# Performance work log

Hardware: AMD Instinct MI355X
Metric: run time of the kernel (lower is better)

The kernel has to match this reference:

```python
import jax, jax.numpy as jnp
import numpy as np

# Poincare ball, curvature c = 1. Assumed manifold ops (standard hyperbolic-attention
# formulations, matching the hypll-style API used by the module):
#   HLinear(x)                ~ expmap0(logmap0(x) @ W + b)   (tangent-space linear)
#   attention_similarity      ~ (-d_poincare(q,k))/tau + gamma
#   attention_activation      ~ softmax over keys
#   attention_midpoint        ~ Mobius gyromidpoint: 0.5 (x) [sum_k w lam(v) v / sum_k w (lam(v)-1)]
#   cat                       ~ expmap0(concat(logmap0(heads)))

EPS = 1e-6
MAX_TANH_ARG = 1.0 - 1e-5

def _norm(x):
    return jnp.sqrt(jnp.clip(jnp.sum(x * x, axis=-1, keepdims=True), EPS))

def expmap0(v):
    n = _norm(v)
    return jnp.tanh(n) * v / n

def logmap0(x):
    n = _norm(x)
    return jnp.arctanh(jnp.minimum(n, MAX_TANH_ARG)) * x / n

def hlinear(x, W, b):
    return expmap0(logmap0(x) @ W + b)

def pairwise_poincare_dist(q, k):
    # q: [B,H,Sq,D] on ball, k: [B,Sk,D] on ball -> d: [B,H,Sq,Sk]
    qn = jnp.clip(jnp.sum(q * q, axis=-1), 0.0, 1.0 - 1e-5)            # [B,H,Sq]
    kn = jnp.clip(jnp.sum(k * k, axis=-1), 0.0, 1.0 - 1e-5)            # [B,Sk]
    dot = jnp.einsum('bhqd,bkd->bhqk', q, k)                            # GEMM-like
    sq = jnp.clip(qn[..., :, None] + kn[:, None, None, :] - 2.0 * dot, 0.0)
    denom = jnp.clip((1.0 - qn)[..., :, None] * (1.0 - kn)[:, None, None, :], EPS)
    arg = 1.0 + 2.0 * sq / denom
    return jnp.arccosh(jnp.maximum(arg, 1.0 + 1e-7))

def mobius_scalar_mul(r, x):
    n = _norm(x)
    return jnp.tanh(r * jnp.arctanh(jnp.minimum(n, MAX_TANH_ARG))) * x / n


def reference(query, key, value, Wq, bq, Wk, bk, Wv, bv, Wo, bo, scale_tau, scale_gamma):
    # batch_first=True; query/key/value: [B,S,D] points on the Poincare ball
    B, S, D = query.shape
    H = Wq.shape[0]

    # per-head full-dimension query projections, vectorized over heads
    tq = logmap0(query)                                                 # [B,S,D]
    q_h = expmap0(jnp.einsum('bsd,hde->bhse', tq, Wq) + bq[None, :, None, :])  # [B,H,S,D]
    # shared K/V projections (use_separate_kv_per_head=False -> MQA)
    k = hlinear(key, Wk, bk)                                            # [B,S,D]
    v = hlinear(value, Wv, bv)                                          # [B,S,D]

    tau = jnp.exp(-scale_tau[0])          # module passes tau = 1/exp(scale_tau)
    gamma = scale_gamma[0]

    d = pairwise_poincare_dist(q_h, k)                                  # [B,H,Sq,Sk]
    sim = -d / tau + gamma
    w = jax.nn.softmax(sim, axis=-1)                                    # [B,H,Sq,Sk]

    # Mobius gyromidpoint of values, weighted per query
    vn = jnp.clip(jnp.sum(v * v, axis=-1), 0.0, 1.0 - 1e-5)             # [B,Sk]
    lam = 2.0 / (1.0 - vn)                                              # [B,Sk]
    num = jnp.einsum('bhqk,bk,bkd->bhqd', w, lam, v)                    # [B,H,Sq,D]
    den = jnp.einsum('bhqk,bk->bhq', w, lam - 1.0)[..., None]           # [B,H,Sq,1]
    mid = mobius_scalar_mul(0.5, num / jnp.clip(den, EPS))              # [B,H,Sq,D]

    # manifold.cat: tangent-space concat of heads, back to the ball
    t = logmap0(mid)                                                    # [B,H,S,D]
    t = jnp.transpose(t, (0, 2, 1, 3)).reshape(B, S, H * D)             # [B,S,H*D]
    concat = expmap0(t)
    return hlinear(concat, Wo, bo)                                      # [B,S,D]


def setup_inputs() -> dict:
    key0 = jax.random.key(0)
    ks = jax.random.split(key0, 16)
    B, S, D, H = 4, 1024, 512, 8
    proj = lambda k: expmap0(0.02 * jax.random.normal(k, (B, S, D), dtype=jnp.float32))
    w_init = lambda k, shape, fan_in: (jax.random.normal(k, shape, dtype=jnp.float32) / np.sqrt(fan_in)).astype(jnp.float32)
    return {
        'query': proj(ks[0]),
        'key': proj(ks[1]),
        'value': proj(ks[2]),
        'Wq': w_init(ks[3], (H, D, D), D),
        'bq': 0.01 * jax.random.normal(ks[4], (H, D), dtype=jnp.float32),
        'Wk': w_init(ks[5], (D, D), D),
        'bk': 0.01 * jax.random.normal(ks[6], (D,), dtype=jnp.float32),
        'Wv': w_init(ks[7], (D, D), D),
        'bv': 0.01 * jax.random.normal(ks[8], (D,), dtype=jnp.float32),
        'Wo': w_init(ks[9], (H * D, D), H * D),
        'bo': 0.01 * jax.random.normal(ks[10], (D,), dtype=jnp.float32),
        'scale_tau': jnp.zeros((1,), dtype=jnp.float32),
        'scale_gamma': jnp.zeros((1,), dtype=jnp.float32),
    }
```

## Files before the change

kernel.cpp:

```cpp
#include <hip/hip_runtime.h>
#include <math.h>

constexpr int B_ = 4, S_ = 1024, D_ = 512, H_ = 8;
constexpr float EPS_ = 1e-6f;
constexpr float MAXT = 1.0f - 1e-5f;

typedef __attribute__((ext_vector_type(8))) short bf16x8;
typedef __attribute__((ext_vector_type(4))) float f32x4;

__device__ __forceinline__ ushort f2b(float f) {
    unsigned u = __float_as_uint(f);
    unsigned r = u + 0x7fffu + ((u >> 16) & 1u);
    return (ushort)(r >> 16);
}
__device__ __forceinline__ float b2f(ushort h) {
    return __uint_as_float(((unsigned)h) << 16);
}

__device__ __forceinline__ void async16(const ushort* g, ushort* l) {
    __builtin_amdgcn_global_load_lds(
        (const __attribute__((address_space(1))) unsigned int*)g,
        (__attribute__((address_space(3))) unsigned int*)l, 16, 0, 0);
}

__device__ __forceinline__ float blk_reduce_sum(float v, float* sm) {
    for (int o = 32; o > 0; o >>= 1) v += __shfl_down(v, o, 64);
    int lane = threadIdx.x & 63, wid = threadIdx.x >> 6;
    if (lane == 0) sm[wid] = v;
    __syncthreads();
    if (threadIdx.x == 0) sm[0] = sm[0] + sm[1] + sm[2] + sm[3];
    __syncthreads();
    float r = sm[0];
    __syncthreads();
    return r;
}

constexpr int GC_ABUF = 256 * 32;
constexpr int GC_BUF = (256 + 128) * 32;
constexpr int GC_SH = GC_BUF * 2;

__device__ __forceinline__ void gemm_core256(const ushort* __restrict__ A,
                                             const ushort* __restrict__ B,
                                             int lda, int ldb, int K, int m0, int n0,
                                             ushort* __restrict__ sh, f32x4 acc[4][8]) {
    const int tid = threadIdx.x;
    const int w = tid >> 6, lane = tid & 63;
    const int quad = lane >> 4, lx = lane & 15;
    const int rr = lane >> 2, c = lane & 3;

    const ushort* aP[4];
    int aOff[4];
#pragma unroll
    for (int i = 0; i < 4; i++) {
        int r = w * 64 + i * 16 + rr;
        int q = c ^ ((r >> 1) & 3);
        aP[i] = A + (size_t)(m0 + r) * lda + q * 8;
        aOff[i] = (w * 64 + i * 16) * 32;
    }
    const ushort* bP[2];
    int bOff[2];
#pragma unroll
    for (int i = 0; i < 2; i++) {
        int r = w * 32 + i * 16 + rr;
        int q = c ^ ((r >> 1) & 3);
        bP[i] = B + (size_t)(n0 + r) * ldb + q * 8;
        bOff[i] = GC_ABUF + (w * 32 + i * 16) * 32;
    }

    int raOff[4], rbOff[8];
#pragma unroll
    for (int i = 0; i < 4; i++) {
        int ra = w * 64 + i * 16 + lx;
        raOff[i] = ra * 32 + (quad ^ ((ra >> 1) & 3)) * 8;
    }
#pragma unroll
    for (int j = 0; j < 8; j++) {
        int rb = j * 16 + lx;
        rbOff[j] = GC_ABUF + rb * 32 + (quad ^ ((rb >> 1) & 3)) * 8;
    }
#pragma unroll
    for (int i = 0; i < 4; i++)
#pragma unroll
        for (int j = 0; j < 8; j++) acc[i][j] = (f32x4)(0.0f);

#pragma unroll
    for (int i = 0; i < 4; i++) async16(aP[i], sh + aOff[i]);
#pragma unroll
    for (int i = 0; i < 2; i++) async16(bP[i], sh + bOff[i]);

    const int nsteps = K >> 5;
    for (int s = 0; s < nsteps; s++) {
        ushort* cur = sh + (s & 1) * GC_BUF;
        if (s + 1 < nsteps) {
            ushort* nxt = sh + ((s + 1) & 1) * GC_BUF;
            int k0 = (s + 1) << 5;
#pragma unroll
            for (int i = 0; i < 4; i++) async16(aP[i] + k0, nxt + aOff[i]);
#pragma unroll
            for (int i = 0; i < 2; i++) async16(bP[i] + k0, nxt + bOff[i]);
            asm volatile("s_waitcnt vmcnt(6)" ::: "memory");
        } else {
            asm volatile("s_waitcnt vmcnt(0)" ::: "memory");
        }
        asm volatile("s_barrier" ::: "memory");
        bf16x8 af[4], bfr[8];
#pragma unroll
        for (int i = 0; i < 4; i++) af[i] = *(const bf16x8*)(cur + raOff[i]);
#pragma unroll
        for (int j = 0; j < 8; j++) bfr[j] = *(const bf16x8*)(cur + rbOff[j]);
#pragma unroll
        for (int i = 0; i < 4; i++)
#pragma unroll
            for (int j = 0; j < 8; j++)
                acc[i][j] = __builtin_amdgcn_mfma_f32_16x16x32_bf16(af[i], bfr[j], acc[i][j], 0, 0, 0);
        asm volatile("s_waitcnt lgkmcnt(0)" ::: "memory");
        asm volatile("s_barrier" ::: "memory");
    }
}

__global__ __launch_bounds__(256, 2) void k_gemm_proj_all(const ushort* __restrict__ tq,
                                                          const ushort* __restrict__ tk,
                                                          const ushort* __restrict__ tv,
                                                          const ushort* __restrict__ WqT,
                                                          const ushort* __restrict__ WkT,
                                                          const ushort* __restrict__ WvT,
                                                          const float* __restrict__ bq,
                                                          const float* __restrict__ bk,
                                                          const float* __restrict__ bv,
                                                          ushort* __restrict__ yq,
                                                          ushort* __restrict__ yk,
                                                          ushort* __restrict__ yv) {
    __shared__ ushort sh[GC_SH];
    int z = blockIdx.z;
    const ushort* A;
    const ushort* BT;
    const float* bias;
    ushort* C;
    int remap = 0, h = 0;
    if (z == 0) { A = tk; BT = WkT; bias = bk; C = yk; }
    else if (z == 1) { A = tv; BT = WvT; bias = bv; C = yv; }
    else {
        h = z - 2;
        A = tq; BT = WqT + (size_t)h * 512 * 512; bias = bq + (size_t)h * 512;
        C = yq; remap = 1;
    }
    f32x4 acc[4][8];
    int m0 = blockIdx.y * 256, n0 = blockIdx.x * 128;
    gemm_core256(A, BT, 512, 512, 512, m0, n0, sh, acc);
    int tid = threadIdx.x, w = tid >> 6, lane = tid & 63;
    int quad = lane >> 4, lx = lane & 15;
#pragma unroll
    for (int i = 0; i < 4; i++)
#pragma unroll
        for (int reg = 0; reg < 4; reg++) {
            int m = m0 + w * 64 + i * 16 + quad * 4 + reg;
            size_t orow = remap ? (size_t)((m >> 10) * H_ + h) * S_ + (m & 1023) : (size_t)m;
#pragma unroll
            for (int j = 0; j < 8; j++) {
                int n = n0 + j * 16 + lx;
                C[orow * 512 + n] = f2b(acc[i][j][reg] + bias[n]);
            }
        }
}

__global__ __launch_bounds__(256, 2) void k_gemm_score(const ushort* __restrict__ Aq,
                                                       const ushort* __restrict__ Bk,
                                                       ushort* __restrict__ E,
                                                       float* __restrict__ den,
                                                       const float* __restrict__ qn,
                                                       const float* __restrict__ kn,
                                                       const float* __restrict__ lamM1,
                                                       const float* __restrict__ stau) {
    __shared__ ushort sh[GC_SH];
    int b = blockIdx.z;
    Aq += (size_t)b * 8192 * 512;
    Bk += (size_t)b * 1024 * 512;
    E += (size_t)b * 8192 * 1024;
    den += (size_t)b * 8192;
    qn += (size_t)b * 8192;
    kn += (size_t)b * 1024;
    lamM1 += (size_t)b * 1024;
    f32x4 acc[4][8];
    int m0 = blockIdx.y * 256, n0 = blockIdx.x * 128;
    gemm_core256(Aq, Bk, 512, 512, 512, m0, n0, sh, acc);
    float itau = expf(stau[0]);
    bool tau1 = (itau == 1.0f);
    int tid = threadIdx.x, w_ = tid >> 6, lane = tid & 63;
    int quad = lane >> 4, lx = lane & 15;
    float knv[8], rk[8], lmv[8];
#pragma unroll
    for (int j = 0; j < 8; j++) {
        int n = n0 + j * 16 + lx;
        knv[j] = kn[n];
        rk[j] = __builtin_amdgcn_rcpf(1.0f - knv[j]);
        lmv[j] = lamM1[n];
    }
#pragma unroll
    for (int i = 0; i < 4; i++)
#pragma unroll
        for (int reg = 0; reg < 4; reg++) {
            int m = m0 + w_ * 64 + i * 16 + quad * 4 + reg;
            float q = qn[m];
            float rq2 = 2.0f * __builtin_amdgcn_rcpf(1.0f - q);
            float rsum = 0.0f;
#pragma unroll
            for (int j = 0; j < 8; j++) {
                float dot = acc[i][j][reg];
                float sq = fmaxf(q + knv[j] - 2.0f * dot, 0.0f);
                float rr2 = fminf(rq2 * rk[j], 2e6f);
                float w = fmaxf(sq * rr2, 1e-7f);
                float root = __builtin_amdgcn_sqrtf(__builtin_fmaf(w, w, 2.0f * w));
                float t = 1.0f + w + root;
                float e = tau1 ? __builtin_amdgcn_rcpf(t)
                               : __builtin_amdgcn_exp2f(-itau * __builtin_amdgcn_logf(t));
                ushort eb = f2b(e);
                int n = n0 + j * 16 + lx;
                E[(size_t)m * 1024 + n] = eb;
                rsum += b2f(eb) * lmv[j];
            }
            for (int o = 8; o; o >>= 1) rsum += __shfl_xor(rsum, o, 64);
            if (lx == 0) atomicAdd(&den[m], rsum);
        }
}

__global__ __launch_bounds__(256, 2) void k_gemm_attnv(const ushort* __restrict__ E,
                                                       const ushort* __restrict__ VT,
                                                       const float* __restrict__ den,
                                                       ushort* __restrict__ Ub,
                                                       float* __restrict__ ssU) {
    __shared__ ushort sh[GC_SH];
    int b = blockIdx.z;
    E += (size_t)b * 8192 * 1024;
    VT += (size_t)b * 512 * 1024;
    den += (size_t)b * 8192;
    Ub += (size_t)b * 8192 * 512;
    ssU += (size_t)b * 8192;
    f32x4 acc[4][8];
    int m0 = blockIdx.y * 256, n0 = blockIdx.x * 128;
    gemm_core256(E, VT, 1024, 1024, 1024, m0, n0, sh, acc);
    int tid = threadIdx.x, w = tid >> 6, lane = tid & 63;
    int quad = lane >> 4, lx = lane & 15;
#pragma unroll
    for (int i = 0; i < 4; i++)
#pragma unroll
        for (int reg = 0; reg < 4; reg++) {
            int m = m0 + w * 64 + i * 16 + quad * 4 + reg;
            float inv = __builtin_amdgcn_rcpf(fmaxf(den[m], EPS_));
            float ssum = 0.0f;
#pragma unroll
            for (int j = 0; j < 8; j++) {
                int n = n0 + j * 16 + lx;
                float u = acc[i][j][reg] * inv;
                Ub[(size_t)m * 512 + n] = f2b(u);
                ssum += u * u;
            }
            for (int o = 8; o; o >>= 1) ssum += __shfl_xor(ssum, o, 64);
            if (lx == 0) atomicAdd(&ssU[m], ssum);
        }
}

__global__ __launch_bounds__(256, 2) void k_gemm_sk(const ushort* __restrict__ Ub,
                                                    const ushort* __restrict__ WoT,
                                                    float* __restrict__ Cp) {
    __shared__ ushort sh[GC_SH];
    int z = blockIdx.z;
    int m0 = blockIdx.y * 256, n0 = blockIdx.x * 128;
    int bb = m0 >> 10, s0 = m0 & 1023;
    const ushort* A = Ub + ((size_t)(bb * H_ + z) * S_ + s0) * 512;
    const ushort* BT = WoT + (size_t)z * 512;
    float* C = Cp + (size_t)z * 4096 * 512;
    f32x4 acc[4][8];
    gemm_core256(A, BT, 512, 4096, 512, 0, n0, sh, acc);
    int tid = threadIdx.x, w = tid >> 6, lane = tid & 63;
    int quad = lane >> 4, lx = lane & 15;
#pragma unroll
    for (int i = 0; i < 4; i++)
#pragma unroll
        for (int reg = 0; reg < 4; reg++) {
            int m = m0 + w * 64 + i * 16 + quad * 4 + reg;
#pragma unroll
            for (int j = 0; j < 8; j++) {
                int n = n0 + j * 16 + lx;
                C[(size_t)m * 512 + n] = acc[i][j][reg];
            }
        }
}

__global__ __launch_bounds__(256) void k_hyperfactors(const float* __restrict__ ssU,
                                                      float* __restrict__ Asc8) {
    int idx = blockIdx.x * 256 + threadIdx.x;
    if (idx >= B_ * S_) return;
    int b = idx >> 10, s = idx & 1023;
    float f12[8];
    float sum = 0.0f;
#pragma unroll
    for (int h = 0; h < H_; h++) {
        float ss = ssU[(size_t)(b * H_ + h) * S_ + s];
        float n = sqrtf(fmaxf(ss, EPS_));
        float a = 0.5f * atanhf(fminf(n, MAXT));
        float f1 = tanhf(a) / n;
        float mss = f1 * f1 * ss;
        float nm = sqrtf(fmaxf(mss, EPS_));
        float f2 = atanhf(fminf(nm, MAXT)) / nm;
        f12[h] = f1 * f2;
        sum += f12[h] * f12[h] * ss;
    }
    float nc = sqrtf(fmaxf(sum, EPS_));
    float f3 = tanhf(nc) / nc;
    float css = f3 * f3 * sum;
    float nc2 = sqrtf(fmaxf(css, EPS_));
    float f4 = atanhf(fminf(nc2, MAXT)) / nc2;
    float g = f3 * f4;
#pragma unroll
    for (int h = 0; h < H_; h++) Asc8[(size_t)idx * 8 + h] = f12[h] * g;
}

__global__ __launch_bounds__(256) void k_final_reduce_expmap(const float* __restrict__ Cp,
                                                             const float* __restrict__ Asc8,
                                                             const float* __restrict__ bo,
                                                             float* __restrict__ out) {
    __shared__ float sm[8];
    int r = blockIdx.x;
    float a[8];
#pragma unroll
    for (int z = 0; z < 8; z++) a[z] = Asc8[(size_t)r * 8 + z];
    float v0 = bo[threadIdx.x], v1 = bo[threadIdx.x + 256];
#pragma unroll
    for (int z = 0; z < 8; z++) {
        const float* row = Cp + ((size_t)z * 4096 + r) * 512;
        v0 += a[z] * row[threadIdx.x];
        v1 += a[z] * row[threadIdx.x + 256];
    }
    float ss = blk_reduce_sum(v0 * v0 + v1 * v1, sm);
    float n = sqrtf(fmaxf(ss, EPS_));
    float f = tanhf(n) / n;
    float* o = out + (size_t)r * D_;
    o[threadIdx.x] = f * v0;
    o[threadIdx.x + 256] = f * v1;
}

__global__ __launch_bounds__(256) void k_logmap_bf16(const float* __restrict__ q,
                                                     const float* __restrict__ k,
                                                     const float* __restrict__ v,
                                                     ushort* __restrict__ tq,
                                                     ushort* __restrict__ tk,
                                                     ushort* __restrict__ tv) {
    __shared__ float sm[8];
    const float* x = (blockIdx.y == 0) ? q : (blockIdx.y == 1) ? k : v;
    ushort* t = (blockIdx.y == 0) ? tq : (blockIdx.y == 1) ? tk : tv;
    int r = blockIdx.x;
    const float* xr = x + (size_t)r * D_;
    float v0 = xr[threadIdx.x], v1 = xr[threadIdx.x + 256];
    float ss = blk_reduce_sum(v0 * v0 + v1 * v1, sm);
    float n = sqrtf(fmaxf(ss, EPS_));
    float f = atanhf(fminf(n, MAXT)) / n;
    ushort* tr = t + (size_t)r * D_;
    tr[threadIdx.x] = f2b(f * v0);
    tr[threadIdx.x + 256] = f2b(f * v1);
}

__global__ __launch_bounds__(256) void k_expmap_stats(const ushort* __restrict__ y,
                                                      ushort* __restrict__ outb,
                                                      float* __restrict__ aux, int mode) {
    __shared__ float sm[8];
    int r = blockIdx.x;
    const ushort* yr = y + (size_t)r * D_;
    float v0 = b2f(yr[threadIdx.x]), v1 = b2f(yr[threadIdx.x + 256]);
    float ss = blk_reduce_sum(v0 * v0 + v1 * v1, sm);
    float n = sqrtf(fmaxf(ss, EPS_));
    float f = tanhf(n) / n;
    ushort h0 = f2b(f * v0), h1 = f2b(f * v1);
    float x0 = b2f(h0), x1 = b2f(h1);
    float ss2 = blk_reduce_sum(x0 * x0 + x1 * x1, sm);
    float bn2 = fminf(ss2, MAXT);
    ushort* o = outb + (size_t)r * D_;
    if (mode == 1) {
        o[threadIdx.x] = h0;
        o[threadIdx.x + 256] = h1;
        if (threadIdx.x == 0) aux[r] = bn2;
    } else {
        float lam = 2.0f / (1.0f - bn2);
        o[threadIdx.x] = f2b(lam * x0);
        o[threadIdx.x + 256] = f2b(lam * x1);
        if (threadIdx.x == 0) aux[r] = lam - 1.0f;
    }
}

__global__ __launch_bounds__(256) void k_transpose_f2b(const float* __restrict__ in,
                                                       ushort* __restrict__ out, int R, int C,
                                                       size_t zin, size_t zout) {
    __shared__ float t[32][33];
    in += (size_t)blockIdx.z * zin;
    out += (size_t)blockIdx.z * zout;
    int c0 = blockIdx.x * 32, r0 = blockIdx.y * 32;
    int tx = threadIdx.x & 31, ty = threadIdx.x >> 5;
    for (int rr = ty; rr < 32; rr += 8) t[rr][tx] = in[(size_t)(r0 + rr) * C + c0 + tx];
    __syncthreads();
    for (int rr = ty; rr < 32; rr += 8)
        out[(size_t)(c0 + rr) * R + r0 + tx] = f2b(t[tx][rr]);
}

__global__ __launch_bounds__(256) void k_transpose_b2b(const ushort* __restrict__ in,
                                                       ushort* __restrict__ out, int R, int C,
                                                       size_t zin, size_t zout) {
    __shared__ ushort t[32][34];
    in += (size_t)blockIdx.z * zin;
    out += (size_t)blockIdx.z * zout;
    int c0 = blockIdx.x * 32, r0 = blockIdx.y * 32;
    int tx = threadIdx.x & 31, ty = threadIdx.x >> 5;
    for (int rr = ty; rr < 32; rr += 8) t[rr][tx] = in[(size_t)(r0 + rr) * C + c0 + tx];
    __syncthreads();
    for (int rr = ty; rr < 32; rr += 8)
        out[(size_t)(c0 + rr) * R + r0 + tx] = t[tx][rr];
}

extern "C" void kernel_launch(void* const* d_in, const int* in_sizes, int n_in,
                              void* d_out, int out_size, void* d_ws, size_t ws_size,
                              hipStream_t stream) {
    (void)in_sizes; (void)n_in; (void)out_size; (void)ws_size;
    const float* query = (const float*)d_in[0];
    const float* key = (const float*)d_in[1];
    const float* value = (const float*)d_in[2];
    const float* Wq = (const float*)d_in[3];
    const float* bq = (const float*)d_in[4];
    const float* Wk = (const float*)d_in[5];
    const float* bk = (const float*)d_in[6];
    const float* Wv = (const float*)d_in[7];
    const float* bv = (const float*)d_in[8];
    const float* Wo = (const float*)d_in[9];
    const float* bo = (const float*)d_in[10];
    const float* stau = (const float*)d_in[11];
    float* out = (float*)d_out;

    char* p = (char*)d_ws;
    auto alloc = [&](size_t bytes) {
        char* r = p;
        p += (bytes + 255) & ~(size_t)255;
        return r;
    };
    ushort* tq = (ushort*)alloc((size_t)4096 * 512 * 2);
    ushort* tk = (ushort*)alloc((size_t)4096 * 512 * 2);
    ushort* tv = (ushort*)alloc((size_t)4096 * 512 * 2);
    ushort* WqT = (ushort*)alloc((size_t)8 * 512 * 512 * 2);
    ushort* WkT = (ushort*)alloc((size_t)512 * 512 * 2);
    ushort* WvT = (ushort*)alloc((size_t)512 * 512 * 2);
    ushort* WoT = (ushort*)alloc((size_t)4096 * 512 * 2);
    ushort* yq = (ushort*)alloc((size_t)32768 * 512 * 2);
    ushort* yk = (ushort*)alloc((size_t)4096 * 512 * 2);
    ushort* yv = (ushort*)alloc((size_t)4096 * 512 * 2);
    ushort* qh = (ushort*)alloc((size_t)32768 * 512 * 2);
    ushort* kball = (ushort*)alloc((size_t)4096 * 512 * 2);
    ushort* lamv = (ushort*)alloc((size_t)4096 * 512 * 2);
    ushort* lamvT = (ushort*)alloc((size_t)4 * 512 * 1024 * 2);
    ushort* Sc = (ushort*)alloc((size_t)4 * 8192 * 1024 * 2);
    float* kn = (float*)alloc(4096 * 4);
    float* lamM1 = (float*)alloc(4096 * 4);
    float* qn = (float*)alloc(32768 * 4);
    float* den = (float*)alloc(32768 * 4);
    float* ssU = (float*)alloc(32768 * 4);
    float* Asc8 = (float*)alloc(32768 * 4);
    ushort* Ub = qh;
    float* Cp = (float*)Sc;

    hipMemsetAsync(den, 0, 2 * 32768 * 4, stream);

    k_logmap_bf16<<<dim3(4096, 3), 256, 0, stream>>>(query, key, value, tq, tk, tv);

    k_transpose_f2b<<<dim3(16, 16, 1), 256, 0, stream>>>(Wk, WkT, 512, 512, 0, 0);
    k_transpose_f2b<<<dim3(16, 16, 1), 256, 0, stream>>>(Wv, WvT, 512, 512, 0, 0);
    k_transpose_f2b<<<dim3(16, 16, 8), 256, 0, stream>>>(Wq, WqT, 512, 512, (size_t)512 * 512,
                                                         (size_t)512 * 512);
    k_transpose_f2b<<<dim3(16, 128, 1), 256, 0, stream>>>(Wo, WoT, 4096, 512, 0, 0);

    k_gemm_proj_all<<<dim3(4, 16, 10), 256, 0, stream>>>(tq, tk, tv, WqT, WkT, WvT, bq, bk, bv,
                                                         yq, yk, yv);

    k_expmap_stats<<<4096, 256, 0, stream>>>(yk, kball, kn, 1);
    k_expmap_stats<<<4096, 256, 0, stream>>>(yv, lamv, lamM1, 2);
    k_expmap_stats<<<32768, 256, 0, stream>>>(yq, qh, qn, 1);
    k_transpose_b2b<<<dim3(16, 32, 4), 256, 0, stream>>>(lamv, lamvT, 1024, 512,
                                                         (size_t)1024 * 512, (size_t)512 * 1024);

    k_gemm_score<<<dim3(8, 32, 4), 256, 0, stream>>>(qh, kball, Sc, den, qn, kn, lamM1, stau);
    k_gemm_attnv<<<dim3(4, 32, 4), 256, 0, stream>>>(Sc, lamvT, den, Ub, ssU);

    k_hyperfactors<<<16, 256, 0, stream>>>(ssU, Asc8);

    k_gemm_sk<<<dim3(4, 16, 8), 256, 0, stream>>>(Ub, WoT, Cp);
    k_final_reduce_expmap<<<4096, 256, 0, stream>>>(Cp, Asc8, bo, out);
}
```

Before: 390.1 us.

## Fold expmap row scaling into GEMM epilogues and remap blocks per XCD

Drops the three per-row expmap kernels that wrote ball-space copies of q, k and v. The projection GEMM epilogue now accumulates row sums of squares with atomics, and a tiny kernel turns them into per-row scale factors. The score GEMM applies those factors algebraically to the raw dot products and folds the value lambda factor into the stored weights. It also merges the square weight transposes into one launch and remaps score/attnv block indices so neighbouring tiles share an XCD for L2 reuse. This removes about 100MB of elementwise traffic, but the bf16 rounding points shift and more atomics are added.

```diff
diff --git a/kernel.cpp b/kernel.cpp
--- a/kernel.cpp
+++ b/kernel.cpp
@@ -129,20 +129,24 @@
                                                           const float* __restrict__ bv,
                                                           ushort* __restrict__ yq,
                                                           ushort* __restrict__ yk,
-                                                          ushort* __restrict__ yv) {
+                                                          ushort* __restrict__ yv,
+                                                          float* __restrict__ ssq,
+                                                          float* __restrict__ ssk,
+                                                          float* __restrict__ ssv) {
     __shared__ ushort sh[GC_SH];
     int z = blockIdx.z;
     const ushort* A;
     const ushort* BT;
     const float* bias;
     ushort* C;
+    float* SS;
     int remap = 0, h = 0;
-    if (z == 0) { A = tk; BT = WkT; bias = bk; C = yk; }
-    else if (z == 1) { A = tv; BT = WvT; bias = bv; C = yv; }
+    if (z == 0) { A = tk; BT = WkT; bias = bk; C = yk; SS = ssk; }
+    else if (z == 1) { A = tv; BT = WvT; bias = bv; C = yv; SS = ssv; }
     else {
         h = z - 2;
         A = tq; BT = WqT + (size_t)h * 512 * 512; bias = bq + (size_t)h * 512;
-        C = yq; remap = 1;
+        C = yq; SS = ssq; remap = 1;
     }
     f32x4 acc[4][8];
     int m0 = blockIdx.y * 256, n0 = blockIdx.x * 128;
@@ -155,68 +159,120 @@
         for (int reg = 0; reg < 4; reg++) {
             int m = m0 + w * 64 + i * 16 + quad * 4 + reg;
             size_t orow = remap ? (size_t)((m >> 10) * H_ + h) * S_ + (m & 1023) : (size_t)m;
+            float ssum = 0.0f;
 #pragma unroll
             for (int j = 0; j < 8; j++) {
                 int n = n0 + j * 16 + lx;
-                C[orow * 512 + n] = f2b(acc[i][j][reg] + bias[n]);
+                ushort hb = f2b(acc[i][j][reg] + bias[n]);
+                C[orow * 512 + n] = hb;
+                float yv_ = b2f(hb);
+                ssum += yv_ * yv_;
             }
+            for (int o = 8; o; o >>= 1) ssum += __shfl_xor(ssum, o, 64);
+            if (lx == 0) atomicAdd(&SS[orow], ssum);
         }
 }
 
-__global__ __launch_bounds__(256, 2) void k_gemm_score(const ushort* __restrict__ Aq,
-                                                       const ushort* __restrict__ Bk,
+__global__ __launch_bounds__(256) void k_ballfactors(const float* __restrict__ ssq,
+                                                     const float* __restrict__ ssk,
+                                                     const float* __restrict__ ssv,
+                                                     float* __restrict__ fq,
+                                                     float* __restrict__ qn2,
+                                                     float* __restrict__ fk,
+                                                     float* __restrict__ kn2,
+                                                     float* __restrict__ cv,
+                                                     float* __restrict__ dsc) {
+    int idx = blockIdx.x * 256 + threadIdx.x;
+    if (idx >= 40960) return;
+    float ss;
+    if (idx < 32768) ss = ssq[idx];
+    else if (idx < 36864) ss = ssk[idx - 32768];
+    else ss = ssv[idx - 36864];
+    float n = sqrtf(fmaxf(ss, EPS_));
+    float f = tanhf(n) / n;
+    float bn2 = fminf(f * f * ss, MAXT);
+    if (idx < 32768) {
+        fq[idx] = f;
+        qn2[idx] = bn2;
+    } else if (idx < 36864) {
+        fk[idx - 32768] = f;
+        kn2[idx - 32768] = bn2;
+    } else {
+        int r = idx - 36864;
+        float lam = 2.0f / (1.0f - bn2);
+        float c = f * lam;
+        cv[r] = c;
+        dsc[r] = (lam - 1.0f) / c;
+    }
+}
+
+__global__ __launch_bounds__(256, 2) void k_gemm_score(const ushort* __restrict__ Yq,
+                                                       const ushort* __restrict__ Yk,
                                                        ushort* __restrict__ E,
                                                        float* __restrict__ den,
-                                                       const float* __restrict__ qn,
-                                                       const float* __restrict__ kn,
-                                                       const float* __restrict__ lamM1,
+                                                       const float* __restrict__ fq,
+                                                       const float* __restrict__ qn2,
+                                                       const float* __restrict__ fk,
+                                                       const float* __restrict__ kn2,
+                                                       const float* __restrict__ cv,
+                                                       const float* __restrict__ dsc,
                                                        const float* __restrict__ stau) {
     __shared__ ushort sh[GC_SH];
-    int b = blockIdx.z;
-    Aq += (size_t)b * 8192 * 512;
-    Bk += (size_t)b * 1024 * 512;
+    int lin = blockIdx.x + 8 * blockIdx.y + 256 * blockIdx.z;
+    int xcd = lin & 7, p = lin >> 3;
+    int b = p >> 5, q_ = p & 31;
+    int m0 = (4 * xcd + (q_ >> 3)) * 256;
+    int n0 = (q_ & 7) * 128;
+    const ushort* Aq = Yq + (size_t)b * 8192 * 512;
+    const ushort* Bk = Yk + (size_t)b * 1024 * 512;
     E += (size_t)b * 8192 * 1024;
     den += (size_t)b * 8192;
-    qn += (size_t)b * 8192;
-    kn += (size_t)b * 1024;
-    lamM1 += (size_t)b * 1024;
+    const float* fqb = fq + (size_t)b * 8192;
+    const float* qn2b = qn2 + (size_t)b * 8192;
+    const float* fkb = fk + (size_t)b * 1024;
+    const float* kn2b = kn2 + (size_t)b * 1024;
+    const float* cvb = cv + (size_t)b * 1024;
+    const float* dscb = dsc + (size_t)b * 1024;
+
     f32x4 acc[4][8];
-    int m0 = blockIdx.y * 256, n0 = blockIdx.x * 128;
     gemm_core256(Aq, Bk, 512, 512, 512, m0, n0, sh, acc);
     float itau = expf(stau[0]);
     bool tau1 = (itau == 1.0f);
     int tid = threadIdx.x, w_ = tid >> 6, lane = tid & 63;
     int quad = lane >> 4, lx = lane & 15;
-    float knv[8], rk[8], lmv[8];
+    float fkv[8], kn2v[8], cvv[8], dscv[8], rk[8];
 #pragma unroll
     for (int j = 0; j < 8; j++) {
         int n = n0 + j * 16 + lx;
-        knv[j] = kn[n];
-        rk[j] = __builtin_amdgcn_rcpf(1.0f - knv[j]);
-        lmv[j] = lamM1[n];
+        fkv[j] = fkb[n];
+        kn2v[j] = kn2b[n];
+        rk[j] = __builtin_amdgcn_rcpf(1.0f - kn2v[j]);
+        cvv[j] = cvb[n];
+        dscv[j] = dscb[n];
     }
 #pragma unroll
     for (int i = 0; i < 4; i++)
 #pragma unroll
         for (int reg = 0; reg < 4; reg++) {
             int m = m0 + w_ * 64 + i * 16 + quad * 4 + reg;
-            float q = qn[m];
+            float fqm = fqb[m];
+            float q = qn2b[m];
             float rq2 = 2.0f * __builtin_amdgcn_rcpf(1.0f - q);
             float rsum = 0.0f;
 #pragma unroll
             for (int j = 0; j < 8; j++) {
-                float dot = acc[i][j][reg];
-                float sq = fmaxf(q + knv[j] - 2.0f * dot, 0.0f);
+                float dot = fqm * fkv[j] * acc[i][j][reg];
+                float sq = fmaxf(q + kn2v[j] - 2.0f * dot, 0.0f);
                 float rr2 = fminf(rq2 * rk[j], 2e6f);
                 float w = fmaxf(sq * rr2, 1e-7f);
                 float root = __builtin_amdgcn_sqrtf(__builtin_fmaf(w, w, 2.0f * w));
                 float t = 1.0f + w + root;
                 float e = tau1 ? __builtin_amdgcn_rcpf(t)
                                : __builtin_amdgcn_exp2f(-itau * __builtin_amdgcn_logf(t));
-                ushort eb = f2b(e);
+                ushort eb = f2b(e * cvv[j]);
                 int n = n0 + j * 16 + lx;
                 E[(size_t)m * 1024 + n] = eb;
-                rsum += b2f(eb) * lmv[j];
+                rsum += b2f(eb) * dscv[j];
             }
             for (int o = 8; o; o >>= 1) rsum += __shfl_xor(rsum, o, 64);
             if (lx == 0) atomicAdd(&den[m], rsum);
@@ -229,14 +285,17 @@
                                                        ushort* __restrict__ Ub,
                                                        float* __restrict__ ssU) {
     __shared__ ushort sh[GC_SH];
-    int b = blockIdx.z;
+    int lin = blockIdx.x + 4 * blockIdx.y + 128 * blockIdx.z;
+    int xcd = lin & 7, p = lin >> 3;
+    int b = p >> 4, q_ = p & 15;
+    int m0 = (4 * xcd + (q_ >> 2)) * 256;
+    int n0 = (q_ & 3) * 128;
     E += (size_t)b * 8192 * 1024;
     VT += (size_t)b * 512 * 1024;
     den += (size_t)b * 8192;
     Ub += (size_t)b * 8192 * 512;
     ssU += (size_t)b * 8192;
     f32x4 acc[4][8];
-    int m0 = blockIdx.y * 256, n0 = blockIdx.x * 128;
     gemm_core256(E, VT, 1024, 1024, 1024, m0, n0, sh, acc);
     int tid = threadIdx.x, w = tid >> 6, lane = tid & 63;
     int quad = lane >> 4, lx = lane & 15;
@@ -359,39 +418,30 @@
     tr[threadIdx.x + 256] = f2b(f * v1);
 }
 
-__global__ __launch_bounds__(256) void k_expmap_stats(const ushort* __restrict__ y,
-                                                      ushort* __restrict__ outb,
-                                                      float* __restrict__ aux, int mode) {
-    __shared__ float sm[8];
-    int r = blockIdx.x;
-    const ushort* yr = y + (size_t)r * D_;
-    float v0 = b2f(yr[threadIdx.x]), v1 = b2f(yr[threadIdx.x + 256]);
-    float ss = blk_reduce_sum(v0 * v0 + v1 * v1, sm);
-    float n = sqrtf(fmaxf(ss, EPS_));
-    float f = tanhf(n) / n;
-    ushort h0 = f2b(f * v0), h1 = f2b(f * v1);
-    float x0 = b2f(h0), x1 = b2f(h1);
-    float ss2 = blk_reduce_sum(x0 * x0 + x1 * x1, sm);
-    float bn2 = fminf(ss2, MAXT);
-    ushort* o = outb + (size_t)r * D_;
-    if (mode == 1) {
-        o[threadIdx.x] = h0;
-        o[threadIdx.x + 256] = h1;
-        if (threadIdx.x == 0) aux[r] = bn2;
-    } else {
-        float lam = 2.0f / (1.0f - bn2);
-        o[threadIdx.x] = f2b(lam * x0);
-        o[threadIdx.x + 256] = f2b(lam * x1);
-        if (threadIdx.x == 0) aux[r] = lam - 1.0f;
-    }
+__global__ __launch_bounds__(256) void k_transpose_sqw(const float* __restrict__ Wk,
+                                                       const float* __restrict__ Wv,
+                                                       const float* __restrict__ Wq,
+                                                       ushort* __restrict__ WkT,
+                                                       ushort* __restrict__ WvT,
+                                                       ushort* __restrict__ WqT) {
+    __shared__ float t[32][33];
+    int z = blockIdx.z;
+    const float* in;
+    ushort* out;
+    if (z == 0) { in = Wk; out = WkT; }
+    else if (z == 1) { in = Wv; out = WvT; }
+    else { in = Wq + (size_t)(z - 2) * 512 * 512; out = WqT + (size_t)(z - 2) * 512 * 512; }
+    int c0 = blockIdx.x * 32, r0 = blockIdx.y * 32;
+    int tx = threadIdx.x & 31, ty = threadIdx.x >> 5;
+    for (int rr = ty; rr < 32; rr += 8) t[rr][tx] = in[(size_t)(r0 + rr) * 512 + c0 + tx];
+    __syncthreads();
+    for (int rr = ty; rr < 32; rr += 8)
+        out[(size_t)(c0 + rr) * 512 + r0 + tx] = f2b(t[tx][rr]);
 }
 
 __global__ __launch_bounds__(256) void k_transpose_f2b(const float* __restrict__ in,
-                                                       ushort* __restrict__ out, int R, int C,
-                                                       size_t zin, size_t zout) {
+                                                       ushort* __restrict__ out, int R, int C) {
     __shared__ float t[32][33];
-    in += (size_t)blockIdx.z * zin;
-    out += (size_t)blockIdx.z * zout;
     int c0 = blockIdx.x * 32, r0 = blockIdx.y * 32;
     int tx = threadIdx.x & 31, ty = threadIdx.x >> 5;
     for (int rr = ty; rr < 32; rr += 8) t[rr][tx] = in[(size_t)(r0 + rr) * C + c0 + tx];
@@ -448,41 +498,40 @@
     ushort* yq = (ushort*)alloc((size_t)32768 * 512 * 2);
     ushort* yk = (ushort*)alloc((size_t)4096 * 512 * 2);
     ushort* yv = (ushort*)alloc((size_t)4096 * 512 * 2);
-    ushort* qh = (ushort*)alloc((size_t)32768 * 512 * 2);
-    ushort* kball = (ushort*)alloc((size_t)4096 * 512 * 2);
-    ushort* lamv = (ushort*)alloc((size_t)4096 * 512 * 2);
-    ushort* lamvT = (ushort*)alloc((size_t)4 * 512 * 1024 * 2);
+    ushort* yvT = (ushort*)alloc((size_t)4 * 512 * 1024 * 2);
+    ushort* Ub = (ushort*)alloc((size_t)32768 * 512 * 2);
     ushort* Sc = (ushort*)alloc((size_t)4 * 8192 * 1024 * 2);
-    float* kn = (float*)alloc(4096 * 4);
-    float* lamM1 = (float*)alloc(4096 * 4);
-    float* qn = (float*)alloc(32768 * 4);
     float* den = (float*)alloc(32768 * 4);
     float* ssU = (float*)alloc(32768 * 4);
+    float* ssq = (float*)alloc(32768 * 4);
+    float* ssk = (float*)alloc(4096 * 4);
+    float* ssv = (float*)alloc(4096 * 4);
+    float* fq = (float*)alloc(32768 * 4);
+    float* qn2 = (float*)alloc(32768 * 4);
+    float* fk = (float*)alloc(4096 * 4);
+    float* kn2 = (float*)alloc(4096 * 4);
+    float* cv = (float*)alloc(4096 * 4);
+    float* dsc = (float*)alloc(4096 * 4);
     float* Asc8 = (float*)alloc(32768 * 4);
-    ushort* Ub = qh;
     float* Cp = (float*)Sc;
 
-    hipMemsetAsync(den, 0, 2 * 32768 * 4, stream);
+    hipMemsetAsync(den, 0, (size_t)(32768 * 3 + 4096 * 2 + 192) * 4, stream);
 
     k_logmap_bf16<<<dim3(4096, 3), 256, 0, stream>>>(query, key, value, tq, tk, tv);
 
-    k_transpose_f2b<<<dim3(16, 16, 1), 256, 0, stream>>>(Wk, WkT, 512, 512, 0, 0);
-    k_transpose_f2b<<<dim3(16, 16, 1), 256, 0, stream>>>(Wv, WvT, 512, 512, 0, 0);
-    k_transpose_f2b<<<dim3(16, 16, 8), 256, 0, stream>>>(Wq, WqT, 512, 512, (size_t)512 * 512,
-                                                         (size_t)512 * 512);
-    k_transpose_f2b<<<dim3(16, 128, 1), 256, 0, stream>>>(Wo, WoT, 4096, 512, 0, 0);
+    k_transpose_sqw<<<dim3(16, 16, 10), 256, 0, stream>>>(Wk, Wv, Wq, WkT, WvT, WqT);
+    k_transpose_f2b<<<dim3(16, 128, 1), 256, 0, stream>>>(Wo, WoT, 4096, 512);
 
     k_gemm_proj_all<<<dim3(4, 16, 10), 256, 0, stream>>>(tq, tk, tv, WqT, WkT, WvT, bq, bk, bv,
-                                                         yq, yk, yv);
-
-    k_expmap_stats<<<4096, 256, 0, stream>>>(yk, kball, kn, 1);
-    k_expmap_stats<<<4096, 256, 0, stream>>>(yv, lamv, lamM1, 2);
-    k_expmap_stats<<<32768, 256, 0, stream>>>(yq, qh, qn, 1);
-    k_transpose_b2b<<<dim3(16, 32, 4), 256, 0, stream>>>(lamv, lamvT, 1024, 512,
+                                                         yq, yk, yv, ssq, ssk, ssv);
+
+    k_ballfactors<<<160, 256, 0, stream>>>(ssq, ssk, ssv, fq, qn2, fk, kn2, cv, dsc);
+    k_transpose_b2b<<<dim3(16, 32, 4), 256, 0, stream>>>(yv, yvT, 1024, 512,
                                                          (size_t)1024 * 512, (size_t)512 * 1024);
 
-    k_gemm_score<<<dim3(8, 32, 4), 256, 0, stream>>>(qh, kball, Sc, den, qn, kn, lamM1, stau);
-    k_gemm_attnv<<<dim3(4, 32, 4), 256, 0, stream>>>(Sc, lamvT, den, Ub, ssU);
+    k_gemm_score<<<dim3(8, 32, 4), 256, 0, stream>>>(yq, yk, Sc, den, fq, qn2, fk, kn2, cv, dsc,
+                                                     stau);
+    k_gemm_attnv<<<dim3(4, 32, 4), 256, 0, stream>>>(Sc, yvT, den, Ub, ssU);
 
     k_hyperfactors<<<16, 256, 0, stream>>>(ssU, Asc8);
 
```

New measurement: 364.4 us. 1.07x faster.
